# Performance work log

Measured on AMD Instinct MI355X. Metric: run time of the kernel, lower is better.

The kernel has to match this reference:

```python
import jax, jax.numpy as jnp
import numpy as np

NEG_SLOPE = 0.2  # PyG GATConv default negative_slope


def gat_conv(x, edge_index, W, a_src, a_dst, bias, heads, out_ch, concat):
    """PyG-style GATConv (eval mode, add_self_loops=True).
    x: [N, F_in], edge_index: [2, E] (row 0 = src, row 1 = dst).
    """
    N = x.shape[0]
    loop = jnp.arange(N, dtype=edge_index.dtype)
    src = jnp.concatenate([edge_index[0], loop])  # [E+N]
    dst = jnp.concatenate([edge_index[1], loop])

    h = (x @ W).reshape(N, heads, out_ch)            # [N, H, C]
    alpha_s = jnp.einsum('nhc,hc->nh', h, a_src)     # [N, H]
    alpha_d = jnp.einsum('nhc,hc->nh', h, a_dst)

    e = jax.nn.leaky_relu(alpha_s[src] + alpha_d[dst], NEG_SLOPE)  # [E+N, H]
    # softmax over incoming edges per destination node (numerically stable)
    m = jax.ops.segment_max(e, dst, num_segments=N)                # [N, H]
    ex = jnp.exp(e - m[dst])
    denom = jax.ops.segment_sum(ex, dst, num_segments=N)
    alpha = ex / (denom[dst] + 1e-16)                              # [E+N, H]

    msg = h[src] * alpha[:, :, None]                               # [E+N, H, C]
    out = jax.ops.segment_sum(msg, dst, num_segments=N)            # [N, H, C]
    out = out.reshape(N, heads * out_ch) if concat else out.mean(axis=1)
    return out + bias


def setup_inputs() -> dict:
    key = jax.random.key(0)
    ks = jax.random.split(key, 10)
    N, F_in, H, C1, LAT, E = 10000, 2000, 10, 128, 64, 150000
    hid = H * C1  # 1280
    x = jax.random.normal(ks[0], (N, F_in), dtype=jnp.float32)
    edge_index = jax.random.randint(ks[1], (2, E), 0, N, dtype=jnp.int64)
    # layer 1 params (glorot-ish scaling)
    W1 = jax.random.normal(ks[2], (F_in, H * C1), dtype=jnp.float32) * (1.0 / np.sqrt(F_in))
    a_src1 = jax.random.normal(ks[3], (H, C1), dtype=jnp.float32) * 0.1
    a_dst1 = jax.random.normal(ks[4], (H, C1), dtype=jnp.float32) * 0.1
    b1 = jnp.zeros((hid,), dtype=jnp.float32)
    # layer 2 params
    W2 = jax.random.normal(ks[5], (hid, H * LAT), dtype=jnp.float32) * (1.0 / np.sqrt(hid))
    a_src2 = jax.random.normal(ks[6], (H, LAT), dtype=jnp.float32) * 0.1
    a_dst2 = jax.random.normal(ks[7], (H, LAT), dtype=jnp.float32) * 0.1
    b2 = jnp.zeros((LAT,), dtype=jnp.float32)
    return {"x": x, "edge_index": edge_index,
            "W1": W1, "a_src1": a_src1, "a_dst1": a_dst1, "b1": b1,
            "W2": W2, "a_src2": a_src2, "a_dst2": a_dst2, "b2": b2}


def reference(x, edge_index, W1, a_src1, a_dst1, b1, W2, a_src2, a_dst2, b2):
    H, C1, LAT = 10, 128, 64
    h1 = gat_conv(x, edge_index, W1, a_src1, a_dst1, b1, H, C1, concat=True)
    h1 = jax.nn.relu(h1)
    h2 = gat_conv(h1, edge_index, W2, a_src2, a_dst2, b2, H, LAT, concat=False)
    return jax.nn.relu(h2)
```

## Files before the change

### kernel.cpp

```cpp
#include <hip/hip_runtime.h>

#define NN    10000
#define FIN   2000
#define NH    10
#define C1    128
#define C2    64
#define HC1   1280
#define HC2   640
#define MP    10240
#define K1P   2016

typedef _Float16 f16x8 __attribute__((ext_vector_type(8)));
typedef _Float16 f16x4 __attribute__((ext_vector_type(4)));
typedef _Float16 f16x2 __attribute__((ext_vector_type(2)));
typedef float    f32x4 __attribute__((ext_vector_type(4)));

__device__ __forceinline__ float leaky(float x) { return x > 0.f ? x : 0.2f * x; }

#define NCAST (2 * MP)
#define NW1   (63 * 40)
#define NW2   (40 * 20)
__global__ void k_prep(const float* __restrict__ x, _Float16* __restrict__ A1,
                       const float* __restrict__ W1, _Float16* __restrict__ W1t,
                       const float* __restrict__ W2, _Float16* __restrict__ W2t,
                       const int* __restrict__ ei, int* __restrict__ counts, int E) {
    __shared__ float tile[32][33];
    int bid = blockIdx.x, t = threadIdx.x;
    if (bid < NCAST) {
        int r = bid >> 1;
        int c = (bid & 1) * 256 + t;
        if (c >= K1P / 4) return;
        float4 v = make_float4(0.f, 0.f, 0.f, 0.f);
        if (r < NN && c < FIN / 4) v = *(const float4*)(x + (long)r * FIN + 4 * c);
        f16x4 o = {(_Float16)v.x, (_Float16)v.y, (_Float16)v.z, (_Float16)v.w};
        *(f16x4*)(A1 + (long)r * K1P + 4 * c) = o;
        return;
    }
    const float* W; _Float16* Wt; int K, N, Kpad, kbase, nbase;
    if (bid < NCAST + NW1) {
        int i = bid - NCAST;
        W = W1; Wt = W1t; K = FIN; N = HC1; Kpad = K1P;
        kbase = (i % 63) * 32; nbase = (i / 63) * 32;
    } else if (bid < NCAST + NW1 + NW2) {
        int i = bid - NCAST - NW1;
        W = W2; Wt = W2t; K = HC1; N = HC2; Kpad = HC1;
        kbase = (i % 40) * 32; nbase = (i / 40) * 32;
    } else {
        int e = (bid - NCAST - NW1 - NW2) * 256 + t;
        if (e < E) atomicAdd(&counts[ei[E + e]], 1);
        return;
    }
    int tx = t & 31, ty = t >> 5;
#pragma unroll
    for (int i = 0; i < 4; i++) {
        int k = kbase + ty + i * 8;
        float v = (k < K) ? W[(long)k * N + nbase + tx] : 0.0f;
        tile[ty + i * 8][tx] = v;
    }
    __syncthreads();
#pragma unroll
    for (int i = 0; i < 4; i++) {
        int n = nbase + ty + i * 8;
        Wt[(long)n * Kpad + kbase + tx] = (_Float16)tile[tx][ty + i * 8];
    }
}

__device__ __forceinline__ void gl2lds16(const void* g, void* l) {
    __builtin_amdgcn_global_load_lds((const __attribute__((address_space(1))) void*)g,
                                     (__attribute__((address_space(3))) void*)l, 16, 0, 0);
}

template<int MFRAG>
__global__ __launch_bounds__(256, 3) void k_gemm(const _Float16* __restrict__ A,
                                                 const _Float16* __restrict__ Bt,
                                                 _Float16* __restrict__ C, int K, int N,
                                                 int NTN,
                                                 const float* __restrict__ asf,
                                                 const float* __restrict__ adf,
                                                 float* __restrict__ as,
                                                 float* __restrict__ ad,
                                                 int headw, int nblk,
                                                 const int* __restrict__ ei,
                                                 int* __restrict__ cursor,
                                                 int* __restrict__ colidx, int E) {
    constexpr int BM   = MFRAG * 32;
    constexpr int ABUF = BM * 32;
    constexpr int ASL  = BM / 64;
    constexpr int WVM  = 0x0F70 | (ASL + 2);
    __shared__ char smem[3 * ABUF * 2 + 3 * 8192] __attribute__((aligned(16)));
    _Float16* As = (_Float16*)smem;
    _Float16* Bs = (_Float16*)(smem + 3 * ABUF * 2);

    int bid = blockIdx.x;
    if (bid >= nblk) {
        int i = (bid - nblk) * 256 + threadIdx.x;
        if (i < E + NN) {
            int s, d;
            if (i < E) { s = ei[i]; d = ei[E + i]; }
            else       { s = i - E; d = i - E; }
            int pos = atomicAdd(&cursor[d], 1);
            colidx[pos] = s;
        }
        return;
    }
    int r = bid & 7, qb = bid >> 3;
    int n_t = qb % NTN;
    int m_t = r + 8 * (qb / NTN);
    int m0 = m_t * BM;
    int n0 = n_t * 128;
    int t = threadIdx.x;
    int lane = t & 63, wave = t >> 6;
    int wr = wave >> 1, wc = wave & 1;
    int lrow = lane & 15, q = lane >> 4;

    f32x4 acc[MFRAG][4] = {};

    int sA[ASL], sB[2];
#pragma unroll
    for (int i = 0; i < ASL; i++) sA[i] = t + 256 * i;
#pragma unroll
    for (int i = 0; i < 2; i++) sB[i] = t + 256 * i;
    const _Float16* Ar[ASL];
    const _Float16* Br[2];
#pragma unroll
    for (int i = 0; i < ASL; i++) {
        int row = sA[i] >> 2, gq = (sA[i] & 3) ^ ((sA[i] >> 3) & 3);
        Ar[i] = A + (long)(m0 + row) * K + gq * 8;
    }
#pragma unroll
    for (int i = 0; i < 2; i++) {
        int row = sB[i] >> 2, gq = (sB[i] & 3) ^ ((sB[i] >> 3) & 3);
        Br[i] = Bt + (long)(n0 + row) * K + gq * 8;
    }

    int aoff[MFRAG], boff[4];
#pragma unroll
    for (int i = 0; i < MFRAG; i++) {
        int rowa = wr * (MFRAG * 16) + i * 16 + lrow;
        aoff[i] = rowa * 32 + ((q ^ ((rowa >> 1) & 3)) << 3);
    }
#pragma unroll
    for (int i = 0; i < 4; i++) {
        int rowb = wc * 64 + i * 16 + lrow;
        boff[i] = rowb * 32 + ((q ^ ((rowb >> 1) & 3)) << 3);
    }

    auto stage = [&](int it, int buf) {
        int k0 = it << 5;
#pragma unroll
        for (int i = 0; i < ASL; i++) gl2lds16(Ar[i] + k0, &As[buf * ABUF + sA[i] * 8]);
#pragma unroll
        for (int i = 0; i < 2; i++) gl2lds16(Br[i] + k0, &Bs[buf * 4096 + sB[i] * 8]);
    };

    int nk = K >> 5;
    stage(0, 0);
    stage(1, 1);
    int cur = 0;
    for (int it = 0; it < nk; it++) {
        if (it + 1 < nk) __builtin_amdgcn_s_waitcnt(WVM);
        else             __builtin_amdgcn_s_waitcnt(0x0F70);
        __builtin_amdgcn_s_barrier();
        int nxt = cur + 2; if (nxt >= 3) nxt -= 3;
        if (it + 2 < nk) stage(it + 2, nxt);

        f16x8 af[MFRAG], bf[4];
#pragma unroll
        for (int i = 0; i < MFRAG; i++) af[i] = *(const f16x8*)&As[cur * ABUF + aoff[i]];
#pragma unroll
        for (int i = 0; i < 4; i++) bf[i] = *(const f16x8*)&Bs[cur * 4096 + boff[i]];
#pragma unroll
        for (int mt = 0; mt < MFRAG; mt++)
#pragma unroll
            for (int nt = 0; nt < 4; nt++)
                acc[mt][nt] = __builtin_amdgcn_mfma_f32_16x16x32_f16(bf[nt], af[mt], acc[mt][nt], 0, 0, 0);
        cur = (cur + 1 == 3) ? 0 : cur + 1;
    }

#pragma unroll
    for (int mt = 0; mt < MFRAG; mt++) {
        int m = m0 + wr * (MFRAG * 16) + mt * 16 + lrow;
#pragma unroll
        for (int nt = 0; nt < 4; nt++) {
            int n = n0 + wc * 64 + nt * 16 + q * 4;
            f16x4 o = {(_Float16)acc[mt][nt][0], (_Float16)acc[mt][nt][1],
                       (_Float16)acc[mt][nt][2], (_Float16)acc[mt][nt][3]};
            *(f16x4*)(C + (long)m * N + n) = o;
        }
    }

    float4 av[4], dvv[4];
#pragma unroll
    for (int nt = 0; nt < 4; nt++) {
        av[nt]  = *(const float4*)(asf + n0 + wc * 64 + nt * 16 + q * 4);
        dvv[nt] = *(const float4*)(adf + n0 + wc * 64 + nt * 16 + q * 4);
    }
    __syncthreads();
    float* sAs = (float*)smem;
    float* sAd = (float*)smem + BM * 2;
#pragma unroll
    for (int mt = 0; mt < MFRAG; mt++) {
        float ps = 0.f, pd = 0.f;
#pragma unroll
        for (int nt = 0; nt < 4; nt++) {
            ps += acc[mt][nt][0] * av[nt].x + acc[mt][nt][1] * av[nt].y
                + acc[mt][nt][2] * av[nt].z + acc[mt][nt][3] * av[nt].w;
            pd += acc[mt][nt][0] * dvv[nt].x + acc[mt][nt][1] * dvv[nt].y
                + acc[mt][nt][2] * dvv[nt].z + acc[mt][nt][3] * dvv[nt].w;
        }
        ps += __shfl_xor(ps, 16); ps += __shfl_xor(ps, 32);
        pd += __shfl_xor(pd, 16); pd += __shfl_xor(pd, 32);
        if (q == 0) {
            int rl = wr * (MFRAG * 16) + mt * 16 + lrow;
            sAs[rl * 2 + wc] = ps;
            sAd[rl * 2 + wc] = pd;
        }
    }
    __syncthreads();
    if (t < BM) {
        int m = m0 + t;
        if (m < NN) {
            int hb = n0 / headw;
            if (headw == 128) {
                as[m * NH + hb] = sAs[t * 2] + sAs[t * 2 + 1];
                ad[m * NH + hb] = sAd[t * 2] + sAd[t * 2 + 1];
            } else {
                as[m * NH + hb]     = sAs[t * 2];
                as[m * NH + hb + 1] = sAs[t * 2 + 1];
                ad[m * NH + hb]     = sAd[t * 2];
                ad[m * NH + hb + 1] = sAd[t * 2 + 1];
            }
        }
    }
}

__global__ void k_scan(const int* __restrict__ counts, int* rowptr, int* cursor, int n) {
    __shared__ int s[1024];
    int t = threadIdx.x;
    const int CH = (NN + 1023) / 1024;
    int base = t * CH;
    int loc[CH];
    int sum = 0;
#pragma unroll
    for (int i = 0; i < CH; i++) {
        int idx = base + i;
        int v = (idx < n) ? (counts[idx] + 1) : 0;
        loc[i] = sum;
        sum += v;
    }
    s[t] = sum;
    __syncthreads();
    for (int off = 1; off < 1024; off <<= 1) {
        int add = (t >= off) ? s[t - off] : 0;
        __syncthreads();
        s[t] += add;
        __syncthreads();
    }
    int pre = (t > 0) ? s[t - 1] : 0;
#pragma unroll
    for (int i = 0; i < CH; i++) {
        int idx = base + i;
        if (idx < n) { int ex = pre + loc[i]; rowptr[idx] = ex; cursor[idx] = ex; }
    }
    if (t == 1023) rowptr[n] = s[1023];
}

__global__ __launch_bounds__(320) void k_agg1(const int* __restrict__ rowptr,
                                              const int* __restrict__ colidx,
                                              const float* __restrict__ as,
                                              const float* __restrict__ ad,
                                              const _Float16* __restrict__ h,
                                              const float* __restrict__ bias,
                                              _Float16* __restrict__ A2) {
    __shared__ int sidx[64];
    __shared__ float sal[64 * NH];
    int n = blockIdx.x, t = threadIdx.x;
    if (n >= NN) {
        f16x4 z = {(_Float16)0.f, (_Float16)0.f, (_Float16)0.f, (_Float16)0.f};
        *(f16x4*)(A2 + (long)n * HC1 + 4 * t) = z;
        return;
    }
    int k0 = rowptr[n], deg = rowptr[n + 1] - k0;
    int w = t >> 6, lane = t & 63;
    int hd = t >> 5;
    float acc[4] = {0, 0, 0, 0};

    if (deg <= 64) {
        int src = (lane < deg) ? colidx[k0 + lane] : 0;
        float2 adv = *(const float2*)(ad + n * NH + 2 * w);
        float e0 = -1e30f, e1 = -1e30f;
        if (lane < deg) {
            float2 avv = *(const float2*)(as + (long)src * NH + 2 * w);
            e0 = leaky(avv.x + adv.x);
            e1 = leaky(avv.y + adv.y);
        }
        float m0 = e0, m1 = e1;
        for (int m = 32; m; m >>= 1) {
            m0 = fmaxf(m0, __shfl_xor(m0, m));
            m1 = fmaxf(m1, __shfl_xor(m1, m));
        }
        float x0 = (lane < deg) ? __expf(e0 - m0) : 0.f;
        float x1 = (lane < deg) ? __expf(e1 - m1) : 0.f;
        float s0 = x0, s1 = x1;
        for (int m = 32; m; m >>= 1) {
            s0 += __shfl_xor(s0, m);
            s1 += __shfl_xor(s1, m);
        }
        if (lane < deg) {
            sal[lane * NH + 2 * w]     = x0 / (s0 + 1e-16f);
            sal[lane * NH + 2 * w + 1] = x1 / (s1 + 1e-16f);
            if (w == 0) sidx[lane] = src;
        }
        __syncthreads();
        int j = 0;
        for (; j + 4 <= deg; j += 4) {
            int sj0 = sidx[j], sj1 = sidx[j + 1], sj2 = sidx[j + 2], sj3 = sidx[j + 3];
            float a0 = sal[j * NH + hd], a1 = sal[(j + 1) * NH + hd];
            float a2 = sal[(j + 2) * NH + hd], a3 = sal[(j + 3) * NH + hd];
            f16x4 v0 = *(const f16x4*)(h + (long)sj0 * HC1 + 4 * t);
            f16x4 v1 = *(const f16x4*)(h + (long)sj1 * HC1 + 4 * t);
            f16x4 v2 = *(const f16x4*)(h + (long)sj2 * HC1 + 4 * t);
            f16x4 v3 = *(const f16x4*)(h + (long)sj3 * HC1 + 4 * t);
#pragma unroll
            for (int i = 0; i < 4; i++)
                acc[i] += a0 * (float)v0[i] + a1 * (float)v1[i]
                        + a2 * (float)v2[i] + a3 * (float)v3[i];
        }
        for (; j < deg; j++) {
            int src2 = sidx[j];
            float a = sal[j * NH + hd];
            f16x4 v = *(const f16x4*)(h + (long)src2 * HC1 + 4 * t);
#pragma unroll
            for (int i = 0; i < 4; i++) acc[i] += a * (float)v[i];
        }
    } else {
        float2 adv = *(const float2*)(ad + n * NH + 2 * w);
        float m0 = -1e30f, m1 = -1e30f;
        for (int j = lane; j < deg; j += 64) {
            float2 avv = *(const float2*)(as + (long)colidx[k0 + j] * NH + 2 * w);
            m0 = fmaxf(m0, leaky(avv.x + adv.x));
            m1 = fmaxf(m1, leaky(avv.y + adv.y));
        }
        for (int m = 32; m; m >>= 1) {
            m0 = fmaxf(m0, __shfl_xor(m0, m));
            m1 = fmaxf(m1, __shfl_xor(m1, m));
        }
        float s0 = 0.f, s1 = 0.f;
        for (int j = lane; j < deg; j += 64) {
            float2 avv = *(const float2*)(as + (long)colidx[k0 + j] * NH + 2 * w);
            s0 += __expf(leaky(avv.x + adv.x) - m0);
            s1 += __expf(leaky(avv.y + adv.y) - m1);
        }
        for (int m = 32; m; m >>= 1) {
            s0 += __shfl_xor(s0, m);
            s1 += __shfl_xor(s1, m);
        }
        float i0 = 1.f / (s0 + 1e-16f), i1 = 1.f / (s1 + 1e-16f);
        for (int c0 = 0; c0 < deg; c0 += 64) {
            int cn = min(64, deg - c0);
            __syncthreads();
            if (lane < cn) {
                int src = colidx[k0 + c0 + lane];
                float2 avv = *(const float2*)(as + (long)src * NH + 2 * w);
                sal[lane * NH + 2 * w]     = __expf(leaky(avv.x + adv.x) - m0) * i0;
                sal[lane * NH + 2 * w + 1] = __expf(leaky(avv.y + adv.y) - m1) * i1;
                if (w == 0) sidx[lane] = src;
            }
            __syncthreads();
            for (int j = 0; j < cn; j++) {
                int src2 = sidx[j];
                float a = sal[j * NH + hd];
                f16x4 v = *(const f16x4*)(h + (long)src2 * HC1 + 4 * t);
#pragma unroll
                for (int i = 0; i < 4; i++) acc[i] += a * (float)v[i];
            }
        }
    }
    f16x4 o;
#pragma unroll
    for (int i = 0; i < 4; i++) {
        float x = acc[i] + bias[4 * t + i];
        o[i] = (_Float16)(x > 0.f ? x : 0.f);
    }
    *(f16x4*)(A2 + (long)n * HC1 + 4 * t) = o;
}

__global__ __launch_bounds__(320) void k_agg2(const int* __restrict__ rowptr,
                                              const int* __restrict__ colidx,
                                              const float* __restrict__ as,
                                              const float* __restrict__ ad,
                                              const _Float16* __restrict__ h,
                                              const float* __restrict__ bias,
                                              float* __restrict__ out) {
    __shared__ int sidx[64];
    __shared__ float sal[64 * NH];
    __shared__ float facc[HC2];
    int n = blockIdx.x, t = threadIdx.x;
    int k0 = rowptr[n], deg = rowptr[n + 1] - k0;
    int w = t >> 6, lane = t & 63;
    int hd = t >> 5;
    float a0 = 0.f, a1 = 0.f;

    if (deg <= 64) {
        int src = (lane < deg) ? colidx[k0 + lane] : 0;
        float2 adv = *(const float2*)(ad + n * NH + 2 * w);
        float e0 = -1e30f, e1 = -1e30f;
        if (lane < deg) {
            float2 avv = *(const float2*)(as + (long)src * NH + 2 * w);
            e0 = leaky(avv.x + adv.x);
            e1 = leaky(avv.y + adv.y);
        }
        float m0 = e0, m1 = e1;
        for (int m = 32; m; m >>= 1) {
            m0 = fmaxf(m0, __shfl_xor(m0, m));
            m1 = fmaxf(m1, __shfl_xor(m1, m));
        }
        float x0 = (lane < deg) ? __expf(e0 - m0) : 0.f;
        float x1 = (lane < deg) ? __expf(e1 - m1) : 0.f;
        float s0 = x0, s1 = x1;
        for (int m = 32; m; m >>= 1) {
            s0 += __shfl_xor(s0, m);
            s1 += __shfl_xor(s1, m);
        }
        if (lane < deg) {
            sal[lane * NH + 2 * w]     = x0 / (s0 + 1e-16f);
            sal[lane * NH + 2 * w + 1] = x1 / (s1 + 1e-16f);
            if (w == 0) sidx[lane] = src;
        }
        __syncthreads();
        int j = 0;
        for (; j + 4 <= deg; j += 4) {
            int sj0 = sidx[j], sj1 = sidx[j + 1], sj2 = sidx[j + 2], sj3 = sidx[j + 3];
            float b0 = sal[j * NH + hd], b1 = sal[(j + 1) * NH + hd];
            float b2 = sal[(j + 2) * NH + hd], b3 = sal[(j + 3) * NH + hd];
            f16x2 v0 = *(const f16x2*)(h + (long)sj0 * HC2 + 2 * t);
            f16x2 v1 = *(const f16x2*)(h + (long)sj1 * HC2 + 2 * t);
            f16x2 v2 = *(const f16x2*)(h + (long)sj2 * HC2 + 2 * t);
            f16x2 v3 = *(const f16x2*)(h + (long)sj3 * HC2 + 2 * t);
            a0 += b0 * (float)v0[0] + b1 * (float)v1[0] + b2 * (float)v2[0] + b3 * (float)v3[0];
            a1 += b0 * (float)v0[1] + b1 * (float)v1[1] + b2 * (float)v2[1] + b3 * (float)v3[1];
        }
        for (; j < deg; j++) {
            int src2 = sidx[j];
            float a = sal[j * NH + hd];
            f16x2 v = *(const f16x2*)(h + (long)src2 * HC2 + 2 * t);
            a0 += a * (float)v[0];
            a1 += a * (float)v[1];
        }
    } else {
        float2 adv = *(const float2*)(ad + n * NH + 2 * w);
        float m0 = -1e30f, m1 = -1e30f;
        for (int j = lane; j < deg; j += 64) {
            float2 avv = *(const float2*)(as + (long)colidx[k0 + j] * NH + 2 * w);
            m0 = fmaxf(m0, leaky(avv.x + adv.x));
            m1 = fmaxf(m1, leaky(avv.y + adv.y));
        }
        for (int m = 32; m; m >>= 1) {
            m0 = fmaxf(m0, __shfl_xor(m0, m));
            m1 = fmaxf(m1, __shfl_xor(m1, m));
        }
        float s0 = 0.f, s1 = 0.f;
        for (int j = lane; j < deg; j += 64) {
            float2 avv = *(const float2*)(as + (long)colidx[k0 + j] * NH + 2 * w);
            s0 += __expf(leaky(avv.x + adv.x) - m0);
            s1 += __expf(leaky(avv.y + adv.y) - m1);
        }
        for (int m = 32; m; m >>= 1) {
            s0 += __shfl_xor(s0, m);
            s1 += __shfl_xor(s1, m);
        }
        float i0 = 1.f / (s0 + 1e-16f), i1 = 1.f / (s1 + 1e-16f);
        for (int c0 = 0; c0 < deg; c0 += 64) {
            int cn = min(64, deg - c0);
            __syncthreads();
            if (lane < cn) {
                int src = colidx[k0 + c0 + lane];
                float2 avv = *(const float2*)(as + (long)src * NH + 2 * w);
                sal[lane * NH + 2 * w]     = __expf(leaky(avv.x + adv.x) - m0) * i0;
                sal[lane * NH + 2 * w + 1] = __expf(leaky(avv.y + adv.y) - m1) * i1;
                if (w == 0) sidx[lane] = src;
            }
            __syncthreads();
            for (int j = 0; j < cn; j++) {
                int src2 = sidx[j];
                float a = sal[j * NH + hd];
                f16x2 v = *(const f16x2*)(h + (long)src2 * HC2 + 2 * t);
                a0 += a * (float)v[0];
                a1 += a * (float)v[1];
            }
        }
    }
    facc[2 * t] = a0;
    facc[2 * t + 1] = a1;
    __syncthreads();
    if (t < C2) {
        float s = 0.f;
#pragma unroll
        for (int hh = 0; hh < NH; hh++) s += facc[hh * C2 + t];
        s = s * 0.1f + bias[t];
        out[(long)n * C2 + t] = s > 0.f ? s : 0.f;
    }
}

extern "C" void kernel_launch(void* const* d_in, const int* in_sizes, int n_in,
                              void* d_out, int out_size, void* d_ws, size_t ws_size,
                              hipStream_t stream) {
    const float* x      = (const float*)d_in[0];
    const int*   ei     = (const int*)d_in[1];
    const float* W1     = (const float*)d_in[2];
    const float* asrc1  = (const float*)d_in[3];
    const float* adst1  = (const float*)d_in[4];
    const float* b1     = (const float*)d_in[5];
    const float* W2     = (const float*)d_in[6];
    const float* asrc2  = (const float*)d_in[7];
    const float* adst2  = (const float*)d_in[8];
    const float* b2     = (const float*)d_in[9];
    float* out = (float*)d_out;
    const int E  = in_sizes[1] / 2;
    const int EN = E + NN;

    char* base = (char*)d_ws;
    size_t o = 0;
    auto alloc = [&](size_t bytes) { size_t r = o; o += (bytes + 255) & ~(size_t)255; return r; };
    _Float16* A1    = (_Float16*)(base + alloc((size_t)MP * K1P * 2));
    _Float16* W1t   = (_Float16*)(base + alloc((size_t)HC1 * K1P * 2));
    _Float16* A2    = (_Float16*)(base + alloc((size_t)MP * HC1 * 2));
    _Float16* W2t   = (_Float16*)(base + alloc((size_t)HC2 * HC1 * 2));
    _Float16* h1pre = (_Float16*)(base + alloc((size_t)MP * HC1 * 2));
    _Float16* h2pre = (_Float16*)(base + alloc((size_t)MP * HC2 * 2));
    float* as1      = (float*)(base + alloc((size_t)NN * NH * 4));
    float* ad1      = (float*)(base + alloc((size_t)NN * NH * 4));
    float* as2      = (float*)(base + alloc((size_t)NN * NH * 4));
    float* ad2      = (float*)(base + alloc((size_t)NN * NH * 4));
    int* counts     = (int*)(base + alloc((size_t)(NN + 1) * 4));
    int* rowptr     = (int*)(base + alloc((size_t)(NN + 1) * 4));
    int* cursor     = (int*)(base + alloc((size_t)(NN + 1) * 4));
    int* colidx     = (int*)(base + alloc((size_t)EN * 4));
    (void)ws_size; (void)n_in; (void)out_size;

    const int NCNT = (E + 255) / 256;
    const int FILLB = (EN + 255) / 256;
    const int G1 = 8 * (MP / 128 / 8) * (HC1 / 128);
    const int G2 = 8 * (MP / 128 / 8) * (HC2 / 128);

    hipMemsetAsync(counts, 0, (size_t)(NN + 1) * 4, stream);
    k_prep<<<NCAST + NW1 + NW2 + NCNT, 256, 0, stream>>>(x, A1, W1, W1t, W2, W2t, ei, counts, E);
    k_scan<<<1, 1024, 0, stream>>>(counts, rowptr, cursor, NN);
    k_gemm<4><<<G1 + FILLB, 256, 0, stream>>>(A1, W1t, h1pre, K1P, HC1, HC1 / 128,
                                              asrc1, adst1, as1, ad1, C1,
                                              G1, ei, cursor, colidx, E);
    k_agg1<<<MP, 320, 0, stream>>>(rowptr, colidx, as1, ad1, h1pre, b1, A2);
    k_gemm<4><<<G2, 256, 0, stream>>>(A2, W2t, h2pre, HC1, HC2, HC2 / 128,
                                      asrc2, adst2, as2, ad2, C2,
                                      G2, ei, cursor, colidx, E);
    k_agg2<<<NN, 320, 0, stream>>>(rowptr, colidx, as2, ad2, h2pre, b2, out);
}
```

Measured before the change: 385.4 us.

## Add dedicated 256x256-tile layer-1 GEMM with 512 threads and triple buffering

```diff
diff --git a/kernel.cpp b/kernel.cpp
--- a/kernel.cpp
+++ b/kernel.cpp
@@ -68,6 +68,157 @@
 __device__ __forceinline__ void gl2lds16(const void* g, void* l) {
     __builtin_amdgcn_global_load_lds((const __attribute__((address_space(1))) void*)g,
                                      (__attribute__((address_space(3))) void*)l, 16, 0, 0);
+}
+
+__global__ __launch_bounds__(512, 2) void k_gemm1(const _Float16* __restrict__ A,
+                                                  const _Float16* __restrict__ Bt,
+                                                  _Float16* __restrict__ C,
+                                                  const float* __restrict__ asf,
+                                                  const float* __restrict__ adf,
+                                                  float* __restrict__ as,
+                                                  float* __restrict__ ad,
+                                                  int nblk,
+                                                  const int* __restrict__ ei,
+                                                  int* __restrict__ cursor,
+                                                  int* __restrict__ colidx, int E) {
+    constexpr int K    = K1P;
+    constexpr int N    = HC1;
+    constexpr int TBUF = 256 * 32;
+    __shared__ char smem[3 * TBUF * 2 * 2] __attribute__((aligned(16)));
+    _Float16* As = (_Float16*)smem;
+    _Float16* Bs = (_Float16*)(smem + 3 * TBUF * 2);
+
+    int bid = blockIdx.x;
+    if (bid >= nblk) {
+        int i = (bid - nblk) * 512 + threadIdx.x;
+        if (i < E + NN) {
+            int s, d;
+            if (i < E) { s = ei[i]; d = ei[E + i]; }
+            else       { s = i - E; d = i - E; }
+            int pos = atomicAdd(&cursor[d], 1);
+            colidx[pos] = s;
+        }
+        return;
+    }
+    int r = bid & 7, qb = bid >> 3;
+    int n_t = qb % 5;
+    int m_t = r + 8 * (qb / 5);
+    int m0 = m_t * 256;
+    int n0 = n_t * 256;
+    int t = threadIdx.x;
+    int lane = t & 63, wave = t >> 6;
+    int wr = wave >> 2, wc = wave & 3;
+    int lrow = lane & 15, q = lane >> 4;
+
+    f32x4 acc[8][4] = {};
+
+    int sS[2];
+#pragma unroll
+    for (int i = 0; i < 2; i++) sS[i] = t + 512 * i;
+    const _Float16* Ar[2];
+    const _Float16* Br[2];
+#pragma unroll
+    for (int i = 0; i < 2; i++) {
+        int row = sS[i] >> 2, gq = (sS[i] & 3) ^ ((sS[i] >> 3) & 3);
+        Ar[i] = A  + (long)(m0 + row) * K + gq * 8;
+        Br[i] = Bt + (long)(n0 + row) * K + gq * 8;
+    }
+
+    int aoff[8], boff[4];
+#pragma unroll
+    for (int i = 0; i < 8; i++) {
+        int rowa = wr * 128 + i * 16 + lrow;
+        aoff[i] = rowa * 32 + ((q ^ ((rowa >> 1) & 3)) << 3);
+    }
+#pragma unroll
+    for (int i = 0; i < 4; i++) {
+        int rowb = wc * 64 + i * 16 + lrow;
+        boff[i] = rowb * 32 + ((q ^ ((rowb >> 1) & 3)) << 3);
+    }
+
+    auto stage = [&](int it, int buf) {
+        int k0 = it << 5;
+#pragma unroll
+        for (int i = 0; i < 2; i++) gl2lds16(Ar[i] + k0, &As[buf * TBUF + sS[i] * 8]);
+#pragma unroll
+        for (int i = 0; i < 2; i++) gl2lds16(Br[i] + k0, &Bs[buf * TBUF + sS[i] * 8]);
+    };
+
+    constexpr int WVM = 0x0F70 | 4;
+    int nk = K >> 5;
+    stage(0, 0);
+    stage(1, 1);
+    int cur = 0;
+    for (int it = 0; it < nk; it++) {
+        if (it + 1 < nk) __builtin_amdgcn_s_waitcnt(WVM);
+        else             __builtin_amdgcn_s_waitcnt(0x0F70);
+        __builtin_amdgcn_s_barrier();
+        int nxt = cur + 2; if (nxt >= 3) nxt -= 3;
+        if (it + 2 < nk) stage(it + 2, nxt);
+
+        f16x8 af[8], bf[4];
+#pragma unroll
+        for (int i = 0; i < 8; i++) af[i] = *(const f16x8*)&As[cur * TBUF + aoff[i]];
+#pragma unroll
+        for (int i = 0; i < 4; i++) bf[i] = *(const f16x8*)&Bs[cur * TBUF + boff[i]];
+#pragma unroll
+        for (int mt = 0; mt < 8; mt++)
+#pragma unroll
+            for (int nt = 0; nt < 4; nt++)
+                acc[mt][nt] = __builtin_amdgcn_mfma_f32_16x16x32_f16(bf[nt], af[mt], acc[mt][nt], 0, 0, 0);
+        cur = (cur + 1 == 3) ? 0 : cur + 1;
+    }
+
+#pragma unroll
+    for (int mt = 0; mt < 8; mt++) {
+        int m = m0 + wr * 128 + mt * 16 + lrow;
+#pragma unroll
+        for (int nt = 0; nt < 4; nt++) {
+            int n = n0 + wc * 64 + nt * 16 + q * 4;
+            f16x4 o = {(_Float16)acc[mt][nt][0], (_Float16)acc[mt][nt][1],
+                       (_Float16)acc[mt][nt][2], (_Float16)acc[mt][nt][3]};
+            *(f16x4*)(C + (long)m * N + n) = o;
+        }
+    }
+
+    float4 av[4], dvv[4];
+#pragma unroll
+    for (int nt = 0; nt < 4; nt++) {
+        av[nt]  = *(const float4*)(asf + n0 + wc * 64 + nt * 16 + q * 4);
+        dvv[nt] = *(const float4*)(adf + n0 + wc * 64 + nt * 16 + q * 4);
+    }
+    __syncthreads();
+    float* sAs = (float*)smem;
+    float* sAd = (float*)smem + 1024;
+#pragma unroll
+    for (int mt = 0; mt < 8; mt++) {
+        float ps = 0.f, pd = 0.f;
+#pragma unroll
+        for (int nt = 0; nt < 4; nt++) {
+            ps += acc[mt][nt][0] * av[nt].x + acc[mt][nt][1] * av[nt].y
+                + acc[mt][nt][2] * av[nt].z + acc[mt][nt][3] * av[nt].w;
+            pd += acc[mt][nt][0] * dvv[nt].x + acc[mt][nt][1] * dvv[nt].y
+                + acc[mt][nt][2] * dvv[nt].z + acc[mt][nt][3] * dvv[nt].w;
+        }
+        ps += __shfl_xor(ps, 16); ps += __shfl_xor(ps, 32);
+        pd += __shfl_xor(pd, 16); pd += __shfl_xor(pd, 32);
+        if (q == 0) {
+            int rl = wr * 128 + mt * 16 + lrow;
+            sAs[rl * 4 + wc] = ps;
+            sAd[rl * 4 + wc] = pd;
+        }
+    }
+    __syncthreads();
+    if (t < 256) {
+        int m = m0 + t;
+        if (m < NN) {
+            int hb = n0 >> 7;
+            as[m * NH + hb]     = sAs[t * 4 + 0] + sAs[t * 4 + 1];
+            as[m * NH + hb + 1] = sAs[t * 4 + 2] + sAs[t * 4 + 3];
+            ad[m * NH + hb]     = sAd[t * 4 + 0] + sAd[t * 4 + 1];
+            ad[m * NH + hb + 1] = sAd[t * 4 + 2] + sAd[t * 4 + 3];
+        }
+    }
 }
 
 template<int MFRAG>
@@ -539,16 +690,15 @@
     (void)ws_size; (void)n_in; (void)out_size;
 
     const int NCNT = (E + 255) / 256;
-    const int FILLB = (EN + 255) / 256;
-    const int G1 = 8 * (MP / 128 / 8) * (HC1 / 128);
+    const int FILLB = (EN + 511) / 512;
+    const int G1 = 8 * (MP / 256 / 8) * (HC1 / 256);
     const int G2 = 8 * (MP / 128 / 8) * (HC2 / 128);
 
     hipMemsetAsync(counts, 0, (size_t)(NN + 1) * 4, stream);
     k_prep<<<NCAST + NW1 + NW2 + NCNT, 256, 0, stream>>>(x, A1, W1, W1t, W2, W2t, ei, counts, E);
     k_scan<<<1, 1024, 0, stream>>>(counts, rowptr, cursor, NN);
-    k_gemm<4><<<G1 + FILLB, 256, 0, stream>>>(A1, W1t, h1pre, K1P, HC1, HC1 / 128,
-                                              asrc1, adst1, as1, ad1, C1,
-                                              G1, ei, cursor, colidx, E);
+    k_gemm1<<<G1 + FILLB, 512, 0, stream>>>(A1, W1t, h1pre, asrc1, adst1, as1, ad1,
+                                            G1, ei, cursor, colidx, E);
     k_agg1<<<MP, 320, 0, stream>>>(rowptr, colidx, as1, ad1, h1pre, b1, A2);
     k_gemm<4><<<G2, 256, 0, stream>>>(A2, W2t, h2pre, HC1, HC2, HC2 / 128,
                                       asrc2, adst2, as2, ad2, C2,
```

After: 359.1 us. -6.8%, faster.
